# Kernel tuning notes

Measured on AMD Instinct MI355X. Metric: run time of the kernel, lower is better.

## Reference

```python
import jax, jax.numpy as jnp
import numpy as np
from jax import lax

D_MODEL = 1024
D_STATE = 16
D_CONV = 4
EXPAND = 2
DT_RANK = 64
D_INNER = EXPAND * D_MODEL  # 2048
B, L = 2, 2048
LN_EPS = 1e-5


def setup_inputs() -> dict:
    key = jax.random.key(0)
    ks = jax.random.split(key, 8)

    def n(k, shape, s=0.02):
        return jax.random.normal(k, shape, jnp.float32) * s

    # dt_proj bias initialized like mamba_ssm: inverse-softplus of dt in [1e-3, 1e-1]
    dt = jnp.exp(jax.random.uniform(ks[5], (D_INNER,), jnp.float32)
                 * (np.log(0.1) - np.log(0.001)) + np.log(0.001))
    dt_bias = dt + jnp.log(-jnp.expm1(-dt))
    # A_log init: log(1..d_state) per channel (S4D-real init)
    A_init = jnp.tile(jnp.arange(1, D_STATE + 1, dtype=jnp.float32), (D_INNER, 1))

    return {
        "x": jax.random.normal(ks[0], (B, L, D_MODEL), jnp.float32),
        "ln_w": jnp.ones((D_MODEL,), jnp.float32),
        "ln_b": jnp.zeros((D_MODEL,), jnp.float32),
        "in_proj_w": n(ks[1], (2 * D_INNER, D_MODEL)),
        "conv_w": n(ks[2], (D_INNER, D_CONV), 0.1),
        "conv_b": jnp.zeros((D_INNER,), jnp.float32),
        "x_proj_w": n(ks[3], (DT_RANK + 2 * D_STATE, D_INNER)),
        "dt_proj_w": n(ks[4], (D_INNER, DT_RANK), 0.1),
        "dt_proj_b": dt_bias,
        "A_log": jnp.log(A_init),
        "D": jnp.ones((D_INNER,), jnp.float32),
        "out_proj_w": n(ks[6], (D_MODEL, D_INNER)),
    }


def reference(x, ln_w, ln_b, in_proj_w, conv_w, conv_b, x_proj_w,
              dt_proj_w, dt_proj_b, A_log, D, out_proj_w):
    b = x.shape[0]
    # --- pre-norm (LayerNorm) ---
    mu = x.mean(-1, keepdims=True)
    var = jnp.mean(jnp.square(x - mu), axis=-1, keepdims=True)
    xn = (x - mu) * lax.rsqrt(var + LN_EPS) * ln_w + ln_b

    # --- in_proj -> (u, z) ---
    xz = jnp.einsum('bld,ed->ble', xn, in_proj_w)  # (B,L,2*D_INNER)
    u, z = jnp.split(xz, 2, axis=-1)

    # --- causal depthwise conv1d + SiLU ---
    uc = jnp.transpose(u, (0, 2, 1))  # (B, D_INNER, L)
    uc = lax.conv_general_dilated(
        uc, conv_w[:, None, :], window_strides=(1,),
        padding=[(D_CONV - 1, 0)],
        dimension_numbers=('NCH', 'OIH', 'NCH'),
        feature_group_count=D_INNER)
    u = jax.nn.silu(jnp.transpose(uc, (0, 2, 1)) + conv_b)  # (B,L,D_INNER)

    # --- input-dependent dt, B, C ---
    x_dbl = jnp.einsum('bld,ed->ble', u, x_proj_w)  # (B,L,DT_RANK+2*D_STATE)
    dt, Bm, Cm = jnp.split(x_dbl, [DT_RANK, DT_RANK + D_STATE], axis=-1)
    delta = jax.nn.softplus(jnp.einsum('blr,dr->bld', dt, dt_proj_w) + dt_proj_b)

    # --- selective scan ---
    A = -jnp.exp(A_log)  # (D_INNER, D_STATE)
    dA = jnp.exp(jnp.einsum('bld,dn->bldn', delta, A))          # (B,L,D,N)
    dBu = jnp.einsum('bld,bln,bld->bldn', delta, Bm, u)         # (B,L,D,N)

    def step(h, inputs):
        a_t, b_t, c_t = inputs          # (B,D,N), (B,D,N), (B,N)
        h = a_t * h + b_t
        y_t = jnp.einsum('bdn,bn->bd', h, c_t)
        return h, y_t

    h0 = jnp.zeros((b, D_INNER, D_STATE), x.dtype)
    _, ys = lax.scan(step, h0, (dA.transpose(1, 0, 2, 3),
                                dBu.transpose(1, 0, 2, 3),
                                Cm.transpose(1, 0, 2)))  # ys: (L,B,D_INNER)
    y = ys.transpose(1, 0, 2) + u * D  # skip connection via D

    # --- gate + out_proj + residual ---
    y = y * jax.nn.silu(z)
    out = jnp.einsum('bld,ed->ble', y, out_proj_w)
    return out + x
```

## Files before the change

kernel.cpp:

```cpp
#include <hip/hip_runtime.h>
#include <hip/hip_bf16.h>
#include <cstddef>

#define D_MODEL 1024
#define D_STATE 16
#define D_CONV 4
#define DT_RANK 64
#define D_INNER 2048
#define BB 2
#define LL 2048
#define TT (BB * LL)
#define NSEG 64
#define SEGLEN (LL / NSEG)
#define NCHAN (BB * D_INNER)

typedef __bf16 bf16x8 __attribute__((ext_vector_type(8)));
typedef float floatx4 __attribute__((ext_vector_type(4)));
typedef unsigned short ushortx8 __attribute__((ext_vector_type(8)));

__device__ __forceinline__ unsigned short f2bf(float f) {
  unsigned u = __float_as_uint(f);
  unsigned r = u + 0x7FFF + ((u >> 16) & 1);
  return (unsigned short)(r >> 16);
}
__device__ __forceinline__ float b2f(unsigned short v) {
  return __uint_as_float((unsigned)v << 16);
}

__global__ __launch_bounds__(256) void cast_weights_kernel(
    const float* __restrict__ w0, const float* __restrict__ w1,
    const float* __restrict__ w2, const float* __restrict__ w3,
    unsigned short* __restrict__ dst) {
  int i = blockIdx.x * 256 + threadIdx.x;
  const float* src;
  int off;
  if (i < 1048576) { src = w0; off = 0; }
  else if (i < 1572864) { src = w1; off = 1048576; }
  else if (i < 1622016) { src = w2; off = 1572864; }
  else if (i < 1654784) { src = w3; off = 1622016; }
  else return;
  float4 v = reinterpret_cast<const float4*>(src)[i - off];
  ushort4 o;
  o.x = f2bf(v.x); o.y = f2bf(v.y); o.z = f2bf(v.z); o.w = f2bf(v.w);
  reinterpret_cast<ushort4*>(dst)[i] = o;
}

__global__ __launch_bounds__(256) void cast_dt_kernel(
    const float* __restrict__ xd, unsigned short* __restrict__ dtA) {
  int i = blockIdx.x * 256 + threadIdx.x;
  int row = i >> 4, c = (i & 15) * 4;
  float4 v = *reinterpret_cast<const float4*>(xd + (size_t)row * 96 + c);
  ushort4 o;
  o.x = f2bf(v.x); o.y = f2bf(v.y); o.z = f2bf(v.z); o.w = f2bf(v.w);
  *reinterpret_cast<ushort4*>(dtA + (size_t)row * 64 + c) = o;
}

__global__ __launch_bounds__(256) void layernorm_kernel(
    const float* __restrict__ x, const float* __restrict__ w,
    const float* __restrict__ b, unsigned short* __restrict__ xn) {
  int t = blockIdx.x;
  int tid = threadIdx.x;
  const float4* xr = reinterpret_cast<const float4*>(x + (size_t)t * D_MODEL);
  float4 xv = xr[tid];
  float s = xv.x + xv.y + xv.z + xv.w;
  float sq = xv.x * xv.x + xv.y * xv.y + xv.z * xv.z + xv.w * xv.w;
  for (int off = 32; off >= 1; off >>= 1) {
    s += __shfl_down(s, off);
    sq += __shfl_down(sq, off);
  }
  __shared__ float red[8];
  int wave = tid >> 6;
  if ((tid & 63) == 0) { red[wave * 2] = s; red[wave * 2 + 1] = sq; }
  __syncthreads();
  if (tid == 0) {
    float S = 0.f, Q = 0.f;
    for (int i = 0; i < 4; ++i) { S += red[2 * i]; Q += red[2 * i + 1]; }
    float mean = S * (1.f / D_MODEL);
    float var = Q * (1.f / D_MODEL) - mean * mean;
    red[0] = mean;
    red[1] = rsqrtf(var + 1e-5f);
  }
  __syncthreads();
  float mean = red[0], inv = red[1];
  const float4* wr = reinterpret_cast<const float4*>(w);
  const float4* br = reinterpret_cast<const float4*>(b);
  float4 wv = wr[tid], bv = br[tid];
  ushort4 o;
  o.x = f2bf((xv.x - mean) * inv * wv.x + bv.x);
  o.y = f2bf((xv.y - mean) * inv * wv.y + bv.y);
  o.z = f2bf((xv.z - mean) * inv * wv.z + bv.z);
  o.w = f2bf((xv.w - mean) * inv * wv.w + bv.w);
  reinterpret_cast<ushort4*>(xn + (size_t)t * D_MODEL)[tid] = o;
}

template <int WNF, int EPI, typename OT>
__global__ __launch_bounds__(256) void gemm_bf16_kernel(
    const unsigned short* __restrict__ A, int lda,
    const unsigned short* __restrict__ B, int ldb,
    OT* __restrict__ C, int ldc, int M, int N, int K,
    const float* __restrict__ bias, const float* __restrict__ resid, int ldr,
    unsigned short* __restrict__ C2, int kslice) {
  constexpr int BN = WNF * 32;
  constexpr int BSLOTS = BN * 8;
  constexpr bool NEEDSTAGE = (EPI == 1 || EPI == 4);
  constexpr int TILE_USH = 8192 + BN * 64;
  constexpr int SMEM_USH = NEEDSTAGE && (4 * 64 * 66 > TILE_USH)
                               ? 4 * 64 * 66 : TILE_USH;
  __shared__ unsigned short sm[SMEM_USH];
  unsigned short* Atile = sm;
  unsigned short* Btile = sm + 8192;

  const int tid = threadIdx.x;
  const int lane = tid & 63;
  const int wv = tid >> 6;
  const int wrow = (wv >> 1) * 64;
  const int wcol = (wv & 1) * (WNF * 16);
  int gx = gridDim.x, gy = gridDim.y;
  int lid = blockIdx.y * gx + blockIdx.x;
  int rpx = gy >> 3;
  int xcd = lid & 7;
  int qq0 = lid >> 3;
  int by = xcd * rpx + (qq0 % rpx);
  int bx = qq0 / rpx;
  const int row0 = by * 128;
  const int col0 = bx * BN;
  const int m = lane & 15;
  const int q = lane >> 4;

  int k0lo = 0, k0hi = K;
  if (kslice > 1) {
    int ks = K / kslice;
    k0lo = blockIdx.z * ks;
    k0hi = k0lo + ks;
  }

  floatx4 acc[4][WNF] = {};

  for (int k0 = k0lo; k0 < k0hi; k0 += 64) {
#pragma unroll
    for (int t = 0; t < 4; ++t) {
      int slot = wv * 256 + t * 64 + lane;
      int row = slot >> 3;
      int kg = (slot & 7) ^ (row & 7);
      const unsigned short* ga = A + (size_t)(row0 + row) * lda + k0 + kg * 8;
      __builtin_amdgcn_global_load_lds(
          (const __attribute__((address_space(1))) void*)ga,
          (__attribute__((address_space(3))) void*)(Atile + slot * 8), 16, 0, 0);
    }
#pragma unroll
    for (int t = 0; t < BSLOTS / 256; ++t) {
      int slot = t * 256 + tid;
      int row = slot >> 3;
      int kg = (slot & 7) ^ (row & 7);
      int rowB = col0 + row;
      if (rowB >= N) rowB = N - 1;
      const unsigned short* gb = B + (size_t)rowB * ldb + k0 + kg * 8;
      __builtin_amdgcn_global_load_lds(
          (const __attribute__((address_space(1))) void*)gb,
          (__attribute__((address_space(3))) void*)(Btile + slot * 8), 16, 0, 0);
    }
    __syncthreads();
#pragma unroll
    for (int s = 0; s < 2; ++s) {
      int xr = ((s * 4 + q) ^ (m & 7)) * 8;
      bf16x8 af[4], bfr[WNF];
#pragma unroll
      for (int i = 0; i < 4; ++i)
        af[i] = *reinterpret_cast<const bf16x8*>(
            Atile + (wrow + i * 16 + m) * 64 + xr);
#pragma unroll
      for (int j = 0; j < WNF; ++j)
        bfr[j] = *reinterpret_cast<const bf16x8*>(
            Btile + (wcol + j * 16 + m) * 64 + xr);
#pragma unroll
      for (int i = 0; i < 4; ++i)
#pragma unroll
        for (int j = 0; j < WNF; ++j)
          acc[i][j] = __builtin_amdgcn_mfma_f32_16x16x32_bf16(
              af[i], bfr[j], acc[i][j], 0, 0, 0);
    }
    __syncthreads();
  }

  if (NEEDSTAGE) {
    unsigned short* st = sm + wv * 4224;
    const bool zhalf = (EPI == 4) && (col0 >= D_INNER);
#pragma unroll
    for (int i = 0; i < 4; ++i)
#pragma unroll
      for (int j = 0; j < WNF; ++j)
#pragma unroll
        for (int r = 0; r < 4; ++r) {
          float v = acc[i][j][r];
          if (EPI == 1) {
            float xv = v + bias[col0 + wcol + j * 16 + m];
            v = fmaxf(xv, 0.f) + log1pf(expf(-fabsf(xv)));
          } else if (zhalf) {
            v = v / (1.f + expf(-v));
          }
          st[(i * 16 + q * 4 + r) * 66 + j * 16 + m] = f2bf(v);
        }
    __syncthreads();
    unsigned short* Cb;
    int cb;
    if (EPI == 4 && col0 >= D_INNER) { Cb = C2; cb = col0 - D_INNER + wcol; }
    else { Cb = (unsigned short*)C; cb = col0 + wcol; }
    constexpr int LPR = WNF * 2;
    constexpr int RPI = 64 / LPR;
#pragma unroll
    for (int t = 0; t < 64 / RPI; ++t) {
      int r = t * RPI + lane / LPR;
      int co = (lane % LPR) * 8;
      ushortx8 val = *reinterpret_cast<const ushortx8*>(st + r * 66 + co);
      *reinterpret_cast<ushortx8*>(
          Cb + (size_t)(row0 + wrow + r) * ldc + cb + co) = val;
    }
  } else {
#pragma unroll
    for (int j = 0; j < WNF; ++j) {
      int gc = col0 + wcol + j * 16 + m;
      if (gc >= N) continue;
#pragma unroll
      for (int i = 0; i < 4; ++i) {
#pragma unroll
        for (int r = 0; r < 4; ++r) {
          int gr = row0 + wrow + i * 16 + q * 4 + r;
          float v = acc[i][j][r];
          if (EPI == 2) {
            ((float*)C)[(size_t)gr * ldc + gc] = v + resid[(size_t)gr * ldr + gc];
          } else {
            if (kslice > 1)
              atomicAdd(&((float*)C)[(size_t)gr * ldc + gc], v);
            else
              ((float*)C)[(size_t)gr * ldc + gc] = v;
          }
        }
      }
    }
  }
}

__global__ __launch_bounds__(256) void conv_silu_kernel(
    const unsigned short* __restrict__ ub, const float* __restrict__ cw,
    const float* __restrict__ cb, unsigned short* __restrict__ ucb) {
  size_t idx = (size_t)blockIdx.x * 256 + threadIdx.x;
  if (idx >= (size_t)TT * D_INNER) return;
  int d = (int)(idx & (D_INNER - 1));
  int t = (int)(idx >> 11);
  int l = t & (LL - 1);
  float acc = cb[d];
#pragma unroll
  for (int k = 0; k < D_CONV; ++k) {
    int ll = l - (D_CONV - 1) + k;
    if (ll >= 0)
      acc += b2f(ub[idx - (size_t)(D_CONV - 1 - k) * D_INNER]) * cw[d * D_CONV + k];
  }
  ucb[idx] = f2bf(acc / (1.f + expf(-acc)));
}

__global__ __launch_bounds__(256) void scan_partial_kernel(
    const unsigned short* __restrict__ deltab, const unsigned short* __restrict__ ucb,
    const float* __restrict__ xd, const float* __restrict__ A_log,
    float* __restrict__ aprod_buf, float* __restrict__ hend_buf) {
  __shared__ float Bs[SEGLEN][16];
  const int tid = threadIdx.x;
  const int d = blockIdx.x * 256 + tid;
  const int s = blockIdx.y;
  const int b = blockIdx.z;
  const int chan = b * D_INNER + d;
  const size_t tbase = (size_t)b * LL + (size_t)s * SEGLEN;

  {
    int row = tid >> 3, pair = tid & 7;
    *reinterpret_cast<float2*>(&Bs[row][pair * 2]) =
        *reinterpret_cast<const float2*>(xd + (tbase + row) * 96 + 64 + pair * 2);
  }
  floatx4 Ac[4];
  {
    const floatx4* ar = reinterpret_cast<const floatx4*>(A_log + (size_t)d * D_STATE);
#pragma unroll
    for (int k = 0; k < 4; ++k) {
      floatx4 v = ar[k];
      for (int j = 0; j < 4; ++j) Ac[k][j] = -__expf(v[j]) * 1.4426950408889634f;
    }
  }
  __syncthreads();

  floatx4 h[4] = {};
  float S = 0.f;
  for (int l = 0; l < SEGLEN; ++l) {
    size_t t = tbase + l;
    float dl = b2f(deltab[t * D_INNER + d]);
    float ul = b2f(ucb[t * D_INNER + d]);
    float dlul = dl * ul;
    S += dl;
#pragma unroll
    for (int k = 0; k < 4; ++k) {
      floatx4 bv = *reinterpret_cast<const floatx4*>(&Bs[l][k * 4]);
      floatx4 a;
      for (int j = 0; j < 4; ++j) a[j] = __builtin_amdgcn_exp2f(dl * Ac[k][j]);
      h[k] = a * h[k] + dlul * bv;
    }
  }
  size_t base = ((size_t)s * NCHAN + chan) * D_STATE;
#pragma unroll
  for (int k = 0; k < 4; ++k) {
    floatx4 ap;
    for (int j = 0; j < 4; ++j) ap[j] = __builtin_amdgcn_exp2f(S * Ac[k][j]);
    *reinterpret_cast<floatx4*>(hend_buf + base + k * 4) = h[k];
    *reinterpret_cast<floatx4*>(aprod_buf + base + k * 4) = ap;
  }
}

__global__ __launch_bounds__(256) void scan_combine_kernel(
    float* __restrict__ aprod_buf, const float* __restrict__ hend_buf) {
  int idx = blockIdx.x * 256 + threadIdx.x;
  float H = 0.f;
  for (int s = 0; s < NSEG; ++s) {
    size_t si = (size_t)s * (NCHAN * D_STATE) + idx;
    float a = aprod_buf[si];
    float he = hend_buf[si];
    aprod_buf[si] = H;
    H = he + a * H;
  }
}

__global__ __launch_bounds__(256) void scan_final_kernel(
    const unsigned short* __restrict__ deltab, const unsigned short* __restrict__ ucb,
    const float* __restrict__ xd, const unsigned short* __restrict__ zsb,
    const float* __restrict__ A_log, const float* __restrict__ Dv,
    const float* __restrict__ hstart_buf, unsigned short* __restrict__ yb) {
  __shared__ float BCs[SEGLEN][32];
  const int tid = threadIdx.x;
  const int d = blockIdx.x * 256 + tid;
  const int s = blockIdx.y;
  const int b = blockIdx.z;
  const int chan = b * D_INNER + d;
  const size_t tbase = (size_t)b * LL + (size_t)s * SEGLEN;

  {
    int row = tid >> 3, quad = tid & 7;
    *reinterpret_cast<float4*>(&BCs[row][quad * 4]) =
        *reinterpret_cast<const float4*>(xd + (tbase + row) * 96 + 64 + quad * 4);
  }
  floatx4 Ac[4];
  {
    const floatx4* ar = reinterpret_cast<const floatx4*>(A_log + (size_t)d * D_STATE);
#pragma unroll
    for (int k = 0; k < 4; ++k) {
      floatx4 v = ar[k];
      for (int j = 0; j < 4; ++j) Ac[k][j] = -__expf(v[j]) * 1.4426950408889634f;
    }
  }
  float Dd = Dv[d];
  floatx4 h[4];
  {
    size_t base = ((size_t)s * NCHAN + chan) * D_STATE;
#pragma unroll
    for (int k = 0; k < 4; ++k)
      h[k] = *reinterpret_cast<const floatx4*>(hstart_buf + base + k * 4);
  }
  __syncthreads();

  for (int l = 0; l < SEGLEN; ++l) {
    size_t t = tbase + l;
    float dl = b2f(deltab[t * D_INNER + d]);
    float ul = b2f(ucb[t * D_INNER + d]);
    float dlul = dl * ul;
    floatx4 psum = {};
#pragma unroll
    for (int k = 0; k < 4; ++k) {
      floatx4 bv = *reinterpret_cast<const floatx4*>(&BCs[l][k * 4]);
      floatx4 cv = *reinterpret_cast<const floatx4*>(&BCs[l][16 + k * 4]);
      floatx4 a;
      for (int j = 0; j < 4; ++j) a[j] = __builtin_amdgcn_exp2f(dl * Ac[k][j]);
      h[k] = a * h[k] + dlul * bv;
      psum += h[k] * cv;
    }
    float p = psum[0] + psum[1] + psum[2] + psum[3];
    float zs = b2f(zsb[t * D_INNER + d]);
    yb[t * D_INNER + d] = f2bf((p + ul * Dd) * zs);
  }
}

extern "C" void kernel_launch(void* const* d_in, const int* in_sizes, int n_in,
                              void* d_out, int out_size, void* d_ws, size_t ws_size,
                              hipStream_t stream) {
  const float* x         = (const float*)d_in[0];
  const float* ln_w      = (const float*)d_in[1];
  const float* ln_b      = (const float*)d_in[2];
  const float* in_proj_w = (const float*)d_in[3];
  const float* conv_w    = (const float*)d_in[4];
  const float* conv_b    = (const float*)d_in[5];
  const float* x_proj_w  = (const float*)d_in[6];
  const float* dt_proj_w = (const float*)d_in[7];
  const float* dt_proj_b = (const float*)d_in[8];
  const float* A_log     = (const float*)d_in[9];
  const float* Dvec      = (const float*)d_in[10];
  const float* out_proj_w= (const float*)d_in[11];
  float* out = (float*)d_out;

  unsigned short* wip = (unsigned short*)d_ws;
  unsigned short* wop = wip + 4194304;
  unsigned short* wxp = wop + 2097152;
  unsigned short* wdt = wxp + 196608;
  unsigned short* xnb = wdt + 131072;
  unsigned short* ub  = xnb + (size_t)TT * D_MODEL;
  unsigned short* ucb = ub + (size_t)TT * D_INNER;
  unsigned short* zsb = ucb + (size_t)TT * D_INNER;
  unsigned short* dtA = zsb + (size_t)TT * D_INNER;
  unsigned short* deltab = dtA + (size_t)TT * DT_RANK;
  float* xd    = (float*)(deltab + (size_t)TT * D_INNER);
  float* hend  = xd + (size_t)TT * 96;
  float* aprod = hend + (size_t)NSEG * NCHAN * D_STATE;

  cast_weights_kernel<<<6464, 256, 0, stream>>>(in_proj_w, out_proj_w,
                                                x_proj_w, dt_proj_w, wip);
  hipMemsetAsync(xd, 0, (size_t)TT * 96 * sizeof(float), stream);

  layernorm_kernel<<<TT, 256, 0, stream>>>(x, ln_w, ln_b, xnb);

  gemm_bf16_kernel<4, 4, unsigned short><<<dim3(32, 32), 256, 0, stream>>>(
      xnb, D_MODEL, wip, D_MODEL, ub, D_INNER, TT, 2 * D_INNER, D_MODEL,
      nullptr, nullptr, 0, zsb, 1);

  conv_silu_kernel<<<(TT * D_INNER) / 256, 256, 0, stream>>>(ub, conv_w, conv_b, ucb);

  gemm_bf16_kernel<2, 0, float><<<dim3(2, 32, 4), 256, 0, stream>>>(
      ucb, D_INNER, wxp, D_INNER, xd, 96, TT, 96, D_INNER,
      nullptr, nullptr, 0, nullptr, 4);

  cast_dt_kernel<<<(TT * DT_RANK / 4) / 256, 256, 0, stream>>>(xd, dtA);
  gemm_bf16_kernel<4, 1, unsigned short><<<dim3(16, 32), 256, 0, stream>>>(
      dtA, DT_RANK, wdt, DT_RANK, deltab, D_INNER, TT, D_INNER, DT_RANK,
      dt_proj_b, nullptr, 0, nullptr, 1);

  scan_partial_kernel<<<dim3(D_INNER / 256, NSEG, BB), 256, 0, stream>>>(
      deltab, ucb, xd, A_log, aprod, hend);
  scan_combine_kernel<<<(NCHAN * D_STATE) / 256, 256, 0, stream>>>(aprod, hend);
  scan_final_kernel<<<dim3(D_INNER / 256, NSEG, BB), 256, 0, stream>>>(
      deltab, ucb, xd, zsb, A_log, Dvec, aprod, ucb);

  gemm_bf16_kernel<2, 2, float><<<dim3(16, 32), 256, 0, stream>>>(
      ucb, D_INNER, wop, D_INNER, out, D_MODEL, TT, D_MODEL, D_INNER,
      nullptr, x, D_MODEL, nullptr, 1);
}
```

Before: 362.9 us.

## Fuse prep kernels, fold dt cast into GEMM, vectorize conv, shrink epilogue LDS

```diff
diff --git a/kernel.cpp b/kernel.cpp
--- a/kernel.cpp
+++ b/kernel.cpp
@@ -27,85 +27,75 @@
   return __uint_as_float((unsigned)v << 16);
 }
 
-__global__ __launch_bounds__(256) void cast_weights_kernel(
+__global__ __launch_bounds__(256) void prep_kernel(
+    const float* __restrict__ x, const float* __restrict__ lnw,
+    const float* __restrict__ lnb, unsigned short* __restrict__ xnb,
     const float* __restrict__ w0, const float* __restrict__ w1,
     const float* __restrict__ w2, const float* __restrict__ w3,
-    unsigned short* __restrict__ dst) {
-  int i = blockIdx.x * 256 + threadIdx.x;
+    unsigned short* __restrict__ wdst, float* __restrict__ xd) {
+  const int tid = threadIdx.x;
+  if (blockIdx.x < TT) {
+    int t = blockIdx.x;
+    const float4* xr = reinterpret_cast<const float4*>(x + (size_t)t * D_MODEL);
+    float4 xv = xr[tid];
+    float s = xv.x + xv.y + xv.z + xv.w;
+    float sq = xv.x * xv.x + xv.y * xv.y + xv.z * xv.z + xv.w * xv.w;
+    for (int off = 32; off >= 1; off >>= 1) {
+      s += __shfl_down(s, off);
+      sq += __shfl_down(sq, off);
+    }
+    __shared__ float red[8];
+    int wave = tid >> 6;
+    if ((tid & 63) == 0) { red[wave * 2] = s; red[wave * 2 + 1] = sq; }
+    __syncthreads();
+    if (tid == 0) {
+      float S = 0.f, Q = 0.f;
+      for (int i = 0; i < 4; ++i) { S += red[2 * i]; Q += red[2 * i + 1]; }
+      float mean = S * (1.f / D_MODEL);
+      float var = Q * (1.f / D_MODEL) - mean * mean;
+      red[0] = mean;
+      red[1] = rsqrtf(var + 1e-5f);
+    }
+    __syncthreads();
+    float mean = red[0], inv = red[1];
+    float4 wv = reinterpret_cast<const float4*>(lnw)[tid];
+    float4 bv = reinterpret_cast<const float4*>(lnb)[tid];
+    ushort4 o;
+    o.x = f2bf((xv.x - mean) * inv * wv.x + bv.x);
+    o.y = f2bf((xv.y - mean) * inv * wv.y + bv.y);
+    o.z = f2bf((xv.z - mean) * inv * wv.z + bv.z);
+    o.w = f2bf((xv.w - mean) * inv * wv.w + bv.w);
+    reinterpret_cast<ushort4*>(xnb + (size_t)t * D_MODEL)[tid] = o;
+    return;
+  }
+  int i = (blockIdx.x - TT) * 256 + tid;
   const float* src;
   int off;
   if (i < 1048576) { src = w0; off = 0; }
   else if (i < 1572864) { src = w1; off = 1048576; }
   else if (i < 1622016) { src = w2; off = 1572864; }
   else if (i < 1654784) { src = w3; off = 1622016; }
-  else return;
+  else {
+    float4 zz = {0.f, 0.f, 0.f, 0.f};
+    reinterpret_cast<float4*>(xd)[i - 1654784] = zz;
+    return;
+  }
   float4 v = reinterpret_cast<const float4*>(src)[i - off];
   ushort4 o;
   o.x = f2bf(v.x); o.y = f2bf(v.y); o.z = f2bf(v.z); o.w = f2bf(v.w);
-  reinterpret_cast<ushort4*>(dst)[i] = o;
-}
-
-__global__ __launch_bounds__(256) void cast_dt_kernel(
-    const float* __restrict__ xd, unsigned short* __restrict__ dtA) {
-  int i = blockIdx.x * 256 + threadIdx.x;
-  int row = i >> 4, c = (i & 15) * 4;
-  float4 v = *reinterpret_cast<const float4*>(xd + (size_t)row * 96 + c);
-  ushort4 o;
-  o.x = f2bf(v.x); o.y = f2bf(v.y); o.z = f2bf(v.z); o.w = f2bf(v.w);
-  *reinterpret_cast<ushort4*>(dtA + (size_t)row * 64 + c) = o;
-}
-
-__global__ __launch_bounds__(256) void layernorm_kernel(
-    const float* __restrict__ x, const float* __restrict__ w,
-    const float* __restrict__ b, unsigned short* __restrict__ xn) {
-  int t = blockIdx.x;
-  int tid = threadIdx.x;
-  const float4* xr = reinterpret_cast<const float4*>(x + (size_t)t * D_MODEL);
-  float4 xv = xr[tid];
-  float s = xv.x + xv.y + xv.z + xv.w;
-  float sq = xv.x * xv.x + xv.y * xv.y + xv.z * xv.z + xv.w * xv.w;
-  for (int off = 32; off >= 1; off >>= 1) {
-    s += __shfl_down(s, off);
-    sq += __shfl_down(sq, off);
-  }
-  __shared__ float red[8];
-  int wave = tid >> 6;
-  if ((tid & 63) == 0) { red[wave * 2] = s; red[wave * 2 + 1] = sq; }
-  __syncthreads();
-  if (tid == 0) {
-    float S = 0.f, Q = 0.f;
-    for (int i = 0; i < 4; ++i) { S += red[2 * i]; Q += red[2 * i + 1]; }
-    float mean = S * (1.f / D_MODEL);
-    float var = Q * (1.f / D_MODEL) - mean * mean;
-    red[0] = mean;
-    red[1] = rsqrtf(var + 1e-5f);
-  }
-  __syncthreads();
-  float mean = red[0], inv = red[1];
-  const float4* wr = reinterpret_cast<const float4*>(w);
-  const float4* br = reinterpret_cast<const float4*>(b);
-  float4 wv = wr[tid], bv = br[tid];
-  ushort4 o;
-  o.x = f2bf((xv.x - mean) * inv * wv.x + bv.x);
-  o.y = f2bf((xv.y - mean) * inv * wv.y + bv.y);
-  o.z = f2bf((xv.z - mean) * inv * wv.z + bv.z);
-  o.w = f2bf((xv.w - mean) * inv * wv.w + bv.w);
-  reinterpret_cast<ushort4*>(xn + (size_t)t * D_MODEL)[tid] = o;
-}
-
-template <int WNF, int EPI, typename OT>
+  reinterpret_cast<ushort4*>(wdst)[i] = o;
+}
+
+template <int WNF, int EPI, bool AF32, typename OT>
 __global__ __launch_bounds__(256) void gemm_bf16_kernel(
-    const unsigned short* __restrict__ A, int lda,
+    const void* __restrict__ Ap, int lda,
     const unsigned short* __restrict__ B, int ldb,
     OT* __restrict__ C, int ldc, int M, int N, int K,
     const float* __restrict__ bias, const float* __restrict__ resid, int ldr,
     unsigned short* __restrict__ C2, int kslice) {
   constexpr int BN = WNF * 32;
   constexpr int BSLOTS = BN * 8;
-  constexpr bool NEEDSTAGE = (EPI == 1 || EPI == 4);
-  constexpr int TILE_USH = 8192 + BN * 64;
-  constexpr int SMEM_USH = NEEDSTAGE && (4 * 64 * 66 > TILE_USH)
-                               ? 4 * 64 * 66 : TILE_USH;
+  constexpr int SMEM_USH = 8192 + BN * 64;
   __shared__ unsigned short sm[SMEM_USH];
   unsigned short* Atile = sm;
   unsigned short* Btile = sm + 8192;
@@ -142,10 +132,21 @@
       int slot = wv * 256 + t * 64 + lane;
       int row = slot >> 3;
       int kg = (slot & 7) ^ (row & 7);
-      const unsigned short* ga = A + (size_t)(row0 + row) * lda + k0 + kg * 8;
-      __builtin_amdgcn_global_load_lds(
-          (const __attribute__((address_space(1))) void*)ga,
-          (__attribute__((address_space(3))) void*)(Atile + slot * 8), 16, 0, 0);
+      if (AF32) {
+        const float* ga = (const float*)Ap + (size_t)(row0 + row) * lda + k0 + kg * 8;
+        float4 v0 = *reinterpret_cast<const float4*>(ga);
+        float4 v1 = *reinterpret_cast<const float4*>(ga + 4);
+        ushortx8 pk;
+        pk[0] = f2bf(v0.x); pk[1] = f2bf(v0.y); pk[2] = f2bf(v0.z); pk[3] = f2bf(v0.w);
+        pk[4] = f2bf(v1.x); pk[5] = f2bf(v1.y); pk[6] = f2bf(v1.z); pk[7] = f2bf(v1.w);
+        *reinterpret_cast<ushortx8*>(Atile + slot * 8) = pk;
+      } else {
+        const unsigned short* ga =
+            (const unsigned short*)Ap + (size_t)(row0 + row) * lda + k0 + kg * 8;
+        __builtin_amdgcn_global_load_lds(
+            (const __attribute__((address_space(1))) void*)ga,
+            (__attribute__((address_space(3))) void*)(Atile + slot * 8), 16, 0, 0);
+      }
     }
 #pragma unroll
     for (int t = 0; t < BSLOTS / 256; ++t) {
@@ -182,25 +183,8 @@
     __syncthreads();
   }
 
-  if (NEEDSTAGE) {
-    unsigned short* st = sm + wv * 4224;
+  if (EPI == 1 || EPI == 4) {
     const bool zhalf = (EPI == 4) && (col0 >= D_INNER);
-#pragma unroll
-    for (int i = 0; i < 4; ++i)
-#pragma unroll
-      for (int j = 0; j < WNF; ++j)
-#pragma unroll
-        for (int r = 0; r < 4; ++r) {
-          float v = acc[i][j][r];
-          if (EPI == 1) {
-            float xv = v + bias[col0 + wcol + j * 16 + m];
-            v = fmaxf(xv, 0.f) + log1pf(expf(-fabsf(xv)));
-          } else if (zhalf) {
-            v = v / (1.f + expf(-v));
-          }
-          st[(i * 16 + q * 4 + r) * 66 + j * 16 + m] = f2bf(v);
-        }
-    __syncthreads();
     unsigned short* Cb;
     int cb;
     if (EPI == 4 && col0 >= D_INNER) { Cb = C2; cb = col0 - D_INNER + wcol; }
@@ -208,12 +192,35 @@
     constexpr int LPR = WNF * 2;
     constexpr int RPI = 64 / LPR;
 #pragma unroll
-    for (int t = 0; t < 64 / RPI; ++t) {
-      int r = t * RPI + lane / LPR;
-      int co = (lane % LPR) * 8;
-      ushortx8 val = *reinterpret_cast<const ushortx8*>(st + r * 66 + co);
-      *reinterpret_cast<ushortx8*>(
-          Cb + (size_t)(row0 + wrow + r) * ldc + cb + co) = val;
+    for (int round = 0; round < 2; ++round) {
+      unsigned short* st = sm + wv * 2112;
+      __syncthreads();
+#pragma unroll
+      for (int ii = 0; ii < 2; ++ii) {
+        int i = round * 2 + ii;
+#pragma unroll
+        for (int j = 0; j < WNF; ++j)
+#pragma unroll
+          for (int r = 0; r < 4; ++r) {
+            float v = acc[i][j][r];
+            if (EPI == 1) {
+              float xv = v + bias[col0 + wcol + j * 16 + m];
+              v = fmaxf(xv, 0.f) + log1pf(expf(-fabsf(xv)));
+            } else if (zhalf) {
+              v = v / (1.f + expf(-v));
+            }
+            st[(ii * 16 + q * 4 + r) * 66 + j * 16 + m] = f2bf(v);
+          }
+      }
+      __syncthreads();
+#pragma unroll
+      for (int t = 0; t < 32 / RPI; ++t) {
+        int r = t * RPI + lane / LPR;
+        int co = (lane % LPR) * 8;
+        ushortx8 val = *reinterpret_cast<const ushortx8*>(st + r * 66 + co);
+        *reinterpret_cast<ushortx8*>(
+            Cb + (size_t)(row0 + wrow + round * 32 + r) * ldc + cb + co) = val;
+      }
     }
   } else {
 #pragma unroll
@@ -243,19 +250,32 @@
 __global__ __launch_bounds__(256) void conv_silu_kernel(
     const unsigned short* __restrict__ ub, const float* __restrict__ cw,
     const float* __restrict__ cb, unsigned short* __restrict__ ucb) {
-  size_t idx = (size_t)blockIdx.x * 256 + threadIdx.x;
-  if (idx >= (size_t)TT * D_INNER) return;
-  int d = (int)(idx & (D_INNER - 1));
-  int t = (int)(idx >> 11);
+  size_t i8 = ((size_t)blockIdx.x * 256 + threadIdx.x) * 8;
+  if (i8 >= (size_t)TT * D_INNER) return;
+  int d0 = (int)(i8 & (D_INNER - 1));
+  int t = (int)(i8 >> 11);
   int l = t & (LL - 1);
-  float acc = cb[d];
+  ushortx8 rows[D_CONV];
 #pragma unroll
   for (int k = 0; k < D_CONV; ++k) {
     int ll = l - (D_CONV - 1) + k;
     if (ll >= 0)
-      acc += b2f(ub[idx - (size_t)(D_CONV - 1 - k) * D_INNER]) * cw[d * D_CONV + k];
-  }
-  ucb[idx] = f2bf(acc / (1.f + expf(-acc)));
+      rows[k] = *reinterpret_cast<const ushortx8*>(
+          ub + i8 - (size_t)(D_CONV - 1 - k) * D_INNER);
+    else
+      rows[k] = ushortx8{0, 0, 0, 0, 0, 0, 0, 0};
+  }
+  ushortx8 o;
+#pragma unroll
+  for (int j = 0; j < 8; ++j) {
+    int d = d0 + j;
+    float acc = cb[d];
+#pragma unroll
+    for (int k = 0; k < D_CONV; ++k)
+      acc += b2f(rows[k][j]) * cw[d * D_CONV + k];
+    o[j] = f2bf(acc / (1.f + expf(-acc)));
+  }
+  *reinterpret_cast<ushortx8*>(ucb + i8) = o;
 }
 
 __global__ __launch_bounds__(256) void scan_partial_kernel(
@@ -408,31 +428,28 @@
   unsigned short* ub  = xnb + (size_t)TT * D_MODEL;
   unsigned short* ucb = ub + (size_t)TT * D_INNER;
   unsigned short* zsb = ucb + (size_t)TT * D_INNER;
-  unsigned short* dtA = zsb + (size_t)TT * D_INNER;
-  unsigned short* deltab = dtA + (size_t)TT * DT_RANK;
+  unsigned short* deltab = zsb + (size_t)TT * D_INNER;
   float* xd    = (float*)(deltab + (size_t)TT * D_INNER);
   float* hend  = xd + (size_t)TT * 96;
   float* aprod = hend + (size_t)NSEG * NCHAN * D_STATE;
 
-  cast_weights_kernel<<<6464, 256, 0, stream>>>(in_proj_w, out_proj_w,
-                                                x_proj_w, dt_proj_w, wip);
-  hipMemsetAsync(xd, 0, (size_t)TT * 96 * sizeof(float), stream);
-
-  layernorm_kernel<<<TT, 256, 0, stream>>>(x, ln_w, ln_b, xnb);
-
-  gemm_bf16_kernel<4, 4, unsigned short><<<dim3(32, 32), 256, 0, stream>>>(
+  prep_kernel<<<TT + 6848, 256, 0, stream>>>(x, ln_w, ln_b, xnb, in_proj_w,
+                                             out_proj_w, x_proj_w, dt_proj_w,
+                                             wip, xd);
+
+  gemm_bf16_kernel<4, 4, false, unsigned short><<<dim3(32, 32), 256, 0, stream>>>(
       xnb, D_MODEL, wip, D_MODEL, ub, D_INNER, TT, 2 * D_INNER, D_MODEL,
       nullptr, nullptr, 0, zsb, 1);
 
-  conv_silu_kernel<<<(TT * D_INNER) / 256, 256, 0, stream>>>(ub, conv_w, conv_b, ucb);
-
-  gemm_bf16_kernel<2, 0, float><<<dim3(2, 32, 4), 256, 0, stream>>>(
+  conv_silu_kernel<<<(TT * D_INNER) / (256 * 8), 256, 0, stream>>>(
+      ub, conv_w, conv_b, ucb);
+
+  gemm_bf16_kernel<2, 0, false, float><<<dim3(2, 32, 4), 256, 0, stream>>>(
       ucb, D_INNER, wxp, D_INNER, xd, 96, TT, 96, D_INNER,
       nullptr, nullptr, 0, nullptr, 4);
 
-  cast_dt_kernel<<<(TT * DT_RANK / 4) / 256, 256, 0, stream>>>(xd, dtA);
-  gemm_bf16_kernel<4, 1, unsigned short><<<dim3(16, 32), 256, 0, stream>>>(
-      dtA, DT_RANK, wdt, DT_RANK, deltab, D_INNER, TT, D_INNER, DT_RANK,
+  gemm_bf16_kernel<4, 1, true, unsigned short><<<dim3(16, 32), 256, 0, stream>>>(
+      xd, 96, wdt, DT_RANK, deltab, D_INNER, TT, D_INNER, DT_RANK,
       dt_proj_b, nullptr, 0, nullptr, 1);
 
   scan_partial_kernel<<<dim3(D_INNER / 256, NSEG, BB), 256, 0, stream>>>(
@@ -441,7 +458,7 @@
   scan_final_kernel<<<dim3(D_INNER / 256, NSEG, BB), 256, 0, stream>>>(
       deltab, ucb, xd, zsb, A_log, Dvec, aprod, ucb);
 
-  gemm_bf16_kernel<2, 2, float><<<dim3(16, 32), 256, 0, stream>>>(
+  gemm_bf16_kernel<2, 2, false, float><<<dim3(16, 32), 256, 0, stream>>>(
       ucb, D_INNER, wop, D_INNER, out, D_MODEL, TT, D_MODEL, D_INNER,
       nullptr, x, D_MODEL, nullptr, 1);
 }
```

Result: faster. 336.9 us (-7.1%).
